# Optimization experiments

Hardware: AMD Instinct MI355X
Metric: run time of the kernel (lower is better)

The kernel has to match this reference:

```python
import jax, jax.numpy as jnp
import numpy as np

INP = 256
OUP = 256
FGROUP = 16
CGROUP = 8
K = 3
STRIDE = 1
PAD = K // 2
B, H, W = 16, 64, 64
O1 = OUP * INP * K * K // CGROUP  # 73728, glgf output channels


def setup_inputs() -> dict:
    key = jax.random.key(0)
    ks = jax.random.split(key, 11)
    s = 0.1  # keep sigmoid pre-activations in a sane range
    return {
        "x": jax.random.normal(ks[0], (B, INP, H, W), jnp.float32),
        # GLGF generating the dynamic conv weights (oup*inp*k*k//cgroup outputs)
        "g1_fc1_l": jax.random.normal(ks[1], (INP, INP // FGROUP), jnp.float32) * s,
        "g1_fc1_g1": jax.random.normal(ks[2], (FGROUP, INP // FGROUP), jnp.float32) * s,
        "g1_fc1_g2": jax.random.normal(ks[3], (INP, FGROUP), jnp.float32) * s,
        "g1_fc2_l": jax.random.normal(ks[4], (O1,), jnp.float32) * s,
        "g1_fc2_g": jax.random.normal(ks[5], (INP,), jnp.float32) * s,
        # GLGF generating the per-channel output gate c (oup outputs)
        "g2_fc1_l": jax.random.normal(ks[6], (INP, INP // FGROUP), jnp.float32) * s,
        "g2_fc1_g1": jax.random.normal(ks[7], (FGROUP, INP // FGROUP), jnp.float32) * s,
        "g2_fc1_g2": jax.random.normal(ks[8], (INP, FGROUP), jnp.float32) * s,
        "g2_fc2_l": jax.random.normal(ks[9], (OUP,), jnp.float32) * s,
        "g2_fc2_g": jax.random.normal(ks[10], (INP,), jnp.float32) * s,
    }


def glgf(g, w1l, w1g1, w1g2, w2l, w2g):
    """GLGF applied to a [B, inp] gap vector (all convs are 1x1 -> grouped linears)."""
    b, inp = g.shape
    gp = inp // FGROUP
    gg = g.reshape(b, FGROUP, gp)
    # wn_fc1_l: grouped (fgroup) inp->inp; weight [inp, inp//fgroup]
    local = jnp.einsum('bgi,goi->bgo', gg, w1l.reshape(FGROUP, gp, gp)).reshape(b, inp)
    # wn_fc1_g2(wn_fc1_g1(x)): inp->fgroup (grouped) then fgroup->inp (dense)
    glob = jnp.einsum('bgi,gi->bg', gg, w1g1) @ w1g2.T  # [b, inp]
    h = jax.nn.sigmoid(local + glob)
    # wn_fc2_l: groups=inp, inp->O; weight [O] (1 input channel per output)
    O = w2l.shape[0]
    local2 = (h[:, :, None] * w2l.reshape(inp, O // inp)).reshape(b, O)
    # wn_fc2_g: dense inp->1, broadcast-added
    glob2 = h @ w2g  # [b]
    return local2 + glob2[:, None]


def reference(x, g1_fc1_l, g1_fc1_g1, g1_fc1_g2, g1_fc2_l, g1_fc2_g,
              g2_fc1_l, g2_fc1_g1, g2_fc1_g2, g2_fc2_l, g2_fc2_g):
    b = x.shape[0]
    gap = x.mean(axis=(2, 3))  # adaptive_avg_pool2d to 1x1 -> [b, inp]
    # generate per-sample grouped conv weights: [b, oup, inp//cgroup, k, k]
    xw = glgf(gap, g1_fc1_l, g1_fc1_g1, g1_fc1_g2, g1_fc2_l, g1_fc2_g)
    w = xw.reshape(b, OUP, INP // CGROUP, K, K)
    # torch's groups=b*cgroup batch-trick == per-sample conv with groups=cgroup
    def conv_one(xi, wi):
        return jax.lax.conv_general_dilated(
            xi[None], wi, (STRIDE, STRIDE), [(PAD, PAD), (PAD, PAD)],
            feature_group_count=CGROUP,
            dimension_numbers=('NCHW', 'OIHW', 'NCHW'))[0]
    y = jax.vmap(conv_one)(x, w)  # [b, oup, H, W]
    # per-sample, per-channel gate
    c = glgf(gap, g2_fc1_l, g2_fc1_g1, g2_fc1_g2, g2_fc2_l, g2_fc2_g)  # [b, oup]
    return y * c[:, :, None, None]
```

## Files before the change

### kernel.cpp

```cpp
#include <hip/hip_runtime.h>
#include <cstddef>

typedef __attribute__((ext_vector_type(8))) short bf16x8;
typedef __attribute__((ext_vector_type(4))) unsigned short ushort4v;
typedef __attribute__((ext_vector_type(8))) unsigned short ushort8v;
typedef __attribute__((ext_vector_type(16))) float f32x16;

__device__ __forceinline__ unsigned short f2bf(float f) {
  union { float f; unsigned u; } v; v.f = f;
  unsigned r = v.u + 0x7FFFu + ((v.u >> 16) & 1u);
  return (unsigned short)(r >> 16);
}

#define PADC 132
__global__ __launch_bounds__(256) void prep_kernel(
    const float* __restrict__ x, unsigned short* __restrict__ xt,
    float* __restrict__ partials) {
  __shared__ unsigned short cm[32 * PADC];
  __shared__ float sred[32][32];
  const int bid = blockIdx.x;
  const int wkr = ((bid & 7) << 9) | (bid >> 3);
  const int yp = wkr & 31, g = (wkr >> 5) & 7, b = wkr >> 8;
  const int y0 = yp * 2;
  const int tid = threadIdx.x;
  const float* xg = x + (size_t)(b * 256 + g * 32) * 4096;

  float csum[4];
#pragma unroll
  for (int j = 0; j < 4; ++j) {
    const int idx = tid + 256 * j;
    const int ic = idx >> 5;
    const int r = idx & 31;
    const int ry = r >> 4, gx4 = (r & 15) * 4;
    const float4 v = *reinterpret_cast<const float4*>(
        xg + (size_t)ic * 4096 + (y0 + ry) * 64 + gx4);
    csum[j] = v.x + v.y + v.z + v.w;
    ushort4v s;
    s[0] = f2bf(v.x); s[1] = f2bf(v.y); s[2] = f2bf(v.z); s[3] = f2bf(v.w);
    *reinterpret_cast<ushort4v*>(&cm[ic * PADC + ry * 64 + gx4]) = s;
  }
#pragma unroll
  for (int j = 0; j < 4; ++j) {
    const int ic = (tid >> 5) + 8 * j;
    sred[ic][tid & 31] = csum[j];
  }
  __syncthreads();

  if (tid < 32) {
    float s = 0.f;
#pragma unroll
    for (int i = 0; i < 32; ++i) s += sred[tid][i];
    partials[(size_t)(b * 256 + g * 32 + tid) * 32 + yp] = s;
  }

  const size_t xtb = (size_t)(b * 8 + g) * (66 * 66 * 32);
#pragma unroll
  for (int jj = 0; jj < 2; ++jj) {
    const int o = tid + 256 * jj;
    const int px = o >> 2, icq = o & 3;
    const int ry = px >> 6, gx = px & 63;
    ushort8v t;
#pragma unroll
    for (int c2 = 0; c2 < 8; ++c2) t[c2] = cm[(icq * 8 + c2) * PADC + px];
    *reinterpret_cast<ushort8v*>(
        &xt[xtb + ((size_t)(y0 + ry + 1) * 66 + (gx + 1)) * 32 + icq * 8]) = t;
  }

  const ushort8v z = {0, 0, 0, 0, 0, 0, 0, 0};
  if (tid < 16) {
    const int rr = tid >> 3;
    const int side = (tid >> 2) & 1;
    const int icq = tid & 3;
    const int col = side * 65;
    *reinterpret_cast<ushort8v*>(
        &xt[xtb + ((size_t)(y0 + rr + 1) * 66 + col) * 32 + icq * 8]) = z;
  }
  if (yp == 0 || yp == 31) {
    const int row = (yp == 0) ? 0 : 65;
    for (int o = tid; o < 66 * 4; o += 256) {
      const int col = o >> 2, icq = o & 3;
      *reinterpret_cast<ushort8v*>(
          &xt[xtb + ((size_t)row * 66 + col) * 32 + icq * 8]) = z;
    }
  }
}

__global__ __launch_bounds__(256, 2) void conv_kernel(
    const float* __restrict__ partials,
    const float* __restrict__ w1l, const float* __restrict__ w1g1,
    const float* __restrict__ w1g2, const float* __restrict__ w2l,
    const float* __restrict__ w2g,
    const float* __restrict__ v1l, const float* __restrict__ v1g1,
    const float* __restrict__ v1g2, const float* __restrict__ v2l,
    const float* __restrict__ v2g,
    const unsigned short* __restrict__ xt, float* __restrict__ out) {
  __shared__ __align__(16) unsigned short smem[9216];
  __shared__ float gapL[256];
  __shared__ float hL[256];
  __shared__ float red[256];
  __shared__ float t1L[16];
  __shared__ float gateL[32];

  const int bid = blockIdx.x;
  const int wkr = ((bid & 7) << 7) | (bid >> 3);
  const int yq = wkr & 7;
  const int bg = wkr >> 3;
  const int g = bg & 7, b = bg >> 3;
  const int tid = threadIdx.x;
  const int c = tid;

  {
    float s = 0.f;
    const float* pp = partials + (size_t)(b * 256 + c) * 32;
#pragma unroll
    for (int i = 0; i < 32; ++i) s += pp[i];
    gapL[c] = s * (1.f / 4096.f);
  }
  __syncthreads();

  const int gbase = c & ~15;
  float local1 = 0.f;
#pragma unroll
  for (int i = 0; i < 16; ++i) local1 += gapL[gbase + i] * w1l[c * 16 + i];
  if (c < 16) {
    float t = 0.f;
#pragma unroll
    for (int i = 0; i < 16; ++i) t += gapL[c * 16 + i] * w1g1[c * 16 + i];
    t1L[c] = t;
  }
  __syncthreads();
  float glob1 = 0.f;
#pragma unroll
  for (int gg = 0; gg < 16; ++gg) glob1 += t1L[gg] * w1g2[c * 16 + gg];
  const float h1 = 1.f / (1.f + expf(-(local1 + glob1)));
  hL[c] = h1;
  red[c] = h1 * w2g[c];
  __syncthreads();
  for (int s = 128; s > 0; s >>= 1) {
    if (c < s) red[c] += red[c + s];
    __syncthreads();
  }
  const float glob2 = red[0];
  __syncthreads();

#pragma unroll 4
  for (int it = 0; it < 36; ++it) {
    const int idx = it * 256 + c;
    const int kk = idx >> 9;
    const int rem = idx & 511;
    const int l = rem >> 3, e = rem & 7;
    const int oc = l & 31, hi2 = l >> 5;
    const int ic = ((kk & 1) << 4) + hi2 * 8 + e;
    const int sp = kk >> 1;
    const int o = (g << 5) + oc;
    smem[idx] = f2bf(hL[o] * w2l[o * 288 + ic * 9 + sp] + glob2);
  }
  __syncthreads();

  float local2 = 0.f;
#pragma unroll
  for (int i = 0; i < 16; ++i) local2 += gapL[gbase + i] * v1l[c * 16 + i];
  if (c < 16) {
    float t = 0.f;
#pragma unroll
    for (int i = 0; i < 16; ++i) t += gapL[c * 16 + i] * v1g1[c * 16 + i];
    t1L[c] = t;
  }
  __syncthreads();
  float glob1b = 0.f;
#pragma unroll
  for (int gg = 0; gg < 16; ++gg) glob1b += t1L[gg] * v1g2[c * 16 + gg];
  const float h2 = 1.f / (1.f + expf(-(local2 + glob1b)));
  hL[c] = h2;
  red[c] = h2 * v2g[c];
  __syncthreads();
  for (int s = 128; s > 0; s >>= 1) {
    if (c < s) red[c] += red[c + s];
    __syncthreads();
  }
  if (c < 32) {
    const int o = g * 32 + c;
    gateL[c] = hL[o] * v2l[o] + red[0];
  }

  const int lane = tid & 63, wave = tid >> 6;
  const int n = lane & 31, hi = lane >> 5;
  const int wr = wave >> 1, wc = wave & 1;
  const size_t xtb = (size_t)bg * (66 * 66 * 32);

  bf16x8 a[18];
#pragma unroll
  for (int kk = 0; kk < 18; ++kk) {
    a[kk] = *reinterpret_cast<const bf16x8*>(&smem[kk * 512 + lane * 8]);
    asm volatile("" : "+v"(a[kk]));
  }
  __syncthreads();

  int s_live[5], s_goff[5], s_loff[5];
#pragma unroll
  for (int s = 0; s < 5; ++s) {
    const int li = s * 256 + tid;
    s_live[s] = li < 1056;
    const int r = li / 264;
    const int rem = li - r * 264;
    const int px = rem >> 2, cq = rem & 3;
    s_goff[s] = ((yq * 8 + r) * 66 + px) * 32 + cq * 8;
    s_loff[s] = (((r << 2) + (cq ^ (px & 3))) * 66 + px) * 8;
  }
  ushort8v st[5];

#pragma unroll
  for (int s = 0; s < 5; ++s)
    if (s_live[s])
      st[s] = *reinterpret_cast<const ushort8v*>(&xt[xtb + s_goff[s]]);

#pragma unroll 1
  for (int p = 0; p < 4; ++p) {
#pragma unroll
    for (int s = 0; s < 5; ++s)
      if (s_live[s])
        *reinterpret_cast<ushort8v*>(&smem[s_loff[s]]) = st[s];
    __syncthreads();

    if (p < 3) {
#pragma unroll
      for (int s = 0; s < 5; ++s)
        if (s_live[s])
          st[s] = *reinterpret_cast<const ushort8v*>(
              &xt[xtb + s_goff[s] + (p + 1) * 2 * 66 * 32]);
    }

    f32x16 acc;
#pragma unroll
    for (int i = 0; i < 16; ++i) acc[i] = 0.f;
#pragma unroll
    for (int kk = 0; kk < 18; ++kk) {
      const int sp = kk >> 1;
      const int ky = sp / 3, kx = sp % 3;
      const int px2 = wc * 32 + n + kx;
      const int cq = ((kk & 1) << 1) + hi;
      const bf16x8 bf = *reinterpret_cast<const bf16x8*>(
          &smem[((((wr + ky) << 2) + (cq ^ (px2 & 3))) * 66 + px2) * 8]);
      acc = __builtin_amdgcn_mfma_f32_32x32x16_bf16(a[kk], bf, acc, 0, 0, 0);
    }

    const int y = yq * 8 + p * 2 + wr;
    float* ob = out + (size_t)(b * 256 + g * 32) * 4096 + y * 64 + wc * 32 + n;
#pragma unroll
    for (int r = 0; r < 16; ++r) {
      const int row = (r & 3) + ((r >> 2) << 3) + (hi << 2);
      ob[(size_t)row * 4096] = acc[r] * gateL[row];
    }
    __syncthreads();
  }
}

extern "C" void kernel_launch(void* const* d_in, const int* in_sizes, int n_in,
                              void* d_out, int out_size, void* d_ws,
                              size_t ws_size, hipStream_t stream) {
  const float* x    = (const float*)d_in[0];
  const float* w1l  = (const float*)d_in[1];
  const float* w1g1 = (const float*)d_in[2];
  const float* w1g2 = (const float*)d_in[3];
  const float* w2l  = (const float*)d_in[4];
  const float* w2g  = (const float*)d_in[5];
  const float* v1l  = (const float*)d_in[6];
  const float* v1g1 = (const float*)d_in[7];
  const float* v1g2 = (const float*)d_in[8];
  const float* v2l  = (const float*)d_in[9];
  const float* v2g  = (const float*)d_in[10];
  float* out = (float*)d_out;

  unsigned short* xt = (unsigned short*)d_ws;
  float* partials = (float*)(xt + 17842176);

  prep_kernel<<<4096, 256, 0, stream>>>(x, xt, partials);
  conv_kernel<<<1024, 256, 0, stream>>>(partials, w1l, w1g1, w1g2, w2l, w2g,
                                        v1l, v1g1, v1g2, v2l, v2g, xt, out);
}
```

Measured before the change: 62.27 us.

## Split GLGF weight generation into separate kernel and slim conv kernel

Moves the GLGF weight and gate computation out of the conv kernel into a new 128-block glgf_pack kernel. Each (batch, group) pair is then computed once instead of eight times, and the gate GLGF runs once per batch. The conv kernel now copies prepacked bf16 weights into LDS, reads A fragments from LDS per MFMA instead of holding them in registers, raises the occupancy target to 4, and defers all output stores until after the four row-pair passes. This cuts redundant prologue work and register pressure at the cost of an extra launch, an LDS read per MFMA and a global round trip for the packed weights.

```diff
diff --git a/kernel.cpp b/kernel.cpp
--- a/kernel.cpp
+++ b/kernel.cpp
@@ -85,7 +85,7 @@
   }
 }
 
-__global__ __launch_bounds__(256, 2) void conv_kernel(
+__global__ __launch_bounds__(256) void glgf_pack(
     const float* __restrict__ partials,
     const float* __restrict__ w1l, const float* __restrict__ w1g1,
     const float* __restrict__ w1g2, const float* __restrict__ w2l,
@@ -93,12 +93,93 @@
     const float* __restrict__ v1l, const float* __restrict__ v1g1,
     const float* __restrict__ v1g2, const float* __restrict__ v2l,
     const float* __restrict__ v2g,
-    const unsigned short* __restrict__ xt, float* __restrict__ out) {
-  __shared__ __align__(16) unsigned short smem[9216];
+    unsigned short* __restrict__ wpack, float* __restrict__ gate) {
   __shared__ float gapL[256];
+  __shared__ float t1L[16];
   __shared__ float hL[256];
   __shared__ float red[256];
-  __shared__ float t1L[16];
+  const int bid = blockIdx.x;
+  const int bg = ((bid & 7) << 4) | (bid >> 3);
+  const int g = bg & 7, b = bg >> 3;
+  const int c = threadIdx.x;
+  {
+    float s = 0.f;
+    const float* pp = partials + (size_t)(b * 256 + c) * 32;
+#pragma unroll
+    for (int i = 0; i < 32; ++i) s += pp[i];
+    gapL[c] = s * (1.f / 4096.f);
+  }
+  __syncthreads();
+
+  const int gbase = c & ~15;
+  float local1 = 0.f;
+#pragma unroll
+  for (int i = 0; i < 16; ++i) local1 += gapL[gbase + i] * w1l[c * 16 + i];
+  if (c < 16) {
+    float t = 0.f;
+#pragma unroll
+    for (int i = 0; i < 16; ++i) t += gapL[c * 16 + i] * w1g1[c * 16 + i];
+    t1L[c] = t;
+  }
+  __syncthreads();
+  float glob1 = 0.f;
+#pragma unroll
+  for (int gg = 0; gg < 16; ++gg) glob1 += t1L[gg] * w1g2[c * 16 + gg];
+  const float h1 = 1.f / (1.f + expf(-(local1 + glob1)));
+  hL[c] = h1;
+  red[c] = h1 * w2g[c];
+  __syncthreads();
+  for (int s = 128; s > 0; s >>= 1) {
+    if (c < s) red[c] += red[c + s];
+    __syncthreads();
+  }
+  const float glob2 = red[0];
+
+  unsigned short* wpo = wpack + (size_t)bg * 9216;
+#pragma unroll 4
+  for (int it = 0; it < 36; ++it) {
+    const int idx = it * 256 + c;
+    const int kk = idx >> 9;
+    const int rem = idx & 511;
+    const int l = rem >> 3, e = rem & 7;
+    const int oc = l & 31, hi = l >> 5;
+    const int ic = ((kk & 1) << 4) + hi * 8 + e;
+    const int sp = kk >> 1;
+    const int o = (g << 5) + oc;
+    wpo[idx] = f2bf(hL[o] * w2l[o * 288 + ic * 9 + sp] + glob2);
+  }
+
+  if (g == 0) {
+    __syncthreads();
+    float local2 = 0.f;
+#pragma unroll
+    for (int i = 0; i < 16; ++i) local2 += gapL[gbase + i] * v1l[c * 16 + i];
+    if (c < 16) {
+      float t = 0.f;
+#pragma unroll
+      for (int i = 0; i < 16; ++i) t += gapL[c * 16 + i] * v1g1[c * 16 + i];
+      t1L[c] = t;
+    }
+    __syncthreads();
+    float glob1b = 0.f;
+#pragma unroll
+    for (int gg = 0; gg < 16; ++gg) glob1b += t1L[gg] * v1g2[c * 16 + gg];
+    const float h2 = 1.f / (1.f + expf(-(local2 + glob1b)));
+    red[c] = h2 * v2g[c];
+    __syncthreads();
+    for (int s = 128; s > 0; s >>= 1) {
+      if (c < s) red[c] += red[c + s];
+      __syncthreads();
+    }
+    gate[b * 256 + c] = h2 * v2l[c] + red[0];
+  }
+}
+
+__global__ __launch_bounds__(256, 4) void conv_kernel(
+    const unsigned short* __restrict__ wpack, const float* __restrict__ gate,
+    const unsigned short* __restrict__ xt, float* __restrict__ out) {
+  __shared__ __align__(16) unsigned short wpl[9216];
+  __shared__ __align__(16) unsigned short btile[8448];
   __shared__ float gateL[32];
 
   const int bid = blockIdx.x;
@@ -107,94 +188,19 @@
   const int bg = wkr >> 3;
   const int g = bg & 7, b = bg >> 3;
   const int tid = threadIdx.x;
-  const int c = tid;
-
-  {
-    float s = 0.f;
-    const float* pp = partials + (size_t)(b * 256 + c) * 32;
-#pragma unroll
-    for (int i = 0; i < 32; ++i) s += pp[i];
-    gapL[c] = s * (1.f / 4096.f);
-  }
-  __syncthreads();
-
-  const int gbase = c & ~15;
-  float local1 = 0.f;
-#pragma unroll
-  for (int i = 0; i < 16; ++i) local1 += gapL[gbase + i] * w1l[c * 16 + i];
-  if (c < 16) {
-    float t = 0.f;
-#pragma unroll
-    for (int i = 0; i < 16; ++i) t += gapL[c * 16 + i] * w1g1[c * 16 + i];
-    t1L[c] = t;
-  }
-  __syncthreads();
-  float glob1 = 0.f;
-#pragma unroll
-  for (int gg = 0; gg < 16; ++gg) glob1 += t1L[gg] * w1g2[c * 16 + gg];
-  const float h1 = 1.f / (1.f + expf(-(local1 + glob1)));
-  hL[c] = h1;
-  red[c] = h1 * w2g[c];
-  __syncthreads();
-  for (int s = 128; s > 0; s >>= 1) {
-    if (c < s) red[c] += red[c + s];
-    __syncthreads();
-  }
-  const float glob2 = red[0];
-  __syncthreads();
-
-#pragma unroll 4
-  for (int it = 0; it < 36; ++it) {
-    const int idx = it * 256 + c;
-    const int kk = idx >> 9;
-    const int rem = idx & 511;
-    const int l = rem >> 3, e = rem & 7;
-    const int oc = l & 31, hi2 = l >> 5;
-    const int ic = ((kk & 1) << 4) + hi2 * 8 + e;
-    const int sp = kk >> 1;
-    const int o = (g << 5) + oc;
-    smem[idx] = f2bf(hL[o] * w2l[o * 288 + ic * 9 + sp] + glob2);
-  }
-  __syncthreads();
-
-  float local2 = 0.f;
-#pragma unroll
-  for (int i = 0; i < 16; ++i) local2 += gapL[gbase + i] * v1l[c * 16 + i];
-  if (c < 16) {
-    float t = 0.f;
-#pragma unroll
-    for (int i = 0; i < 16; ++i) t += gapL[c * 16 + i] * v1g1[c * 16 + i];
-    t1L[c] = t;
-  }
-  __syncthreads();
-  float glob1b = 0.f;
-#pragma unroll
-  for (int gg = 0; gg < 16; ++gg) glob1b += t1L[gg] * v1g2[c * 16 + gg];
-  const float h2 = 1.f / (1.f + expf(-(local2 + glob1b)));
-  hL[c] = h2;
-  red[c] = h2 * v2g[c];
-  __syncthreads();
-  for (int s = 128; s > 0; s >>= 1) {
-    if (c < s) red[c] += red[c + s];
-    __syncthreads();
-  }
-  if (c < 32) {
-    const int o = g * 32 + c;
-    gateL[c] = hL[o] * v2l[o] + red[0];
-  }
-
-  const int lane = tid & 63, wave = tid >> 6;
+
+  const int lane = tid & 63;
   const int n = lane & 31, hi = lane >> 5;
+  const int wave = tid >> 6;
   const int wr = wave >> 1, wc = wave & 1;
   const size_t xtb = (size_t)bg * (66 * 66 * 32);
 
-  bf16x8 a[18];
-#pragma unroll
-  for (int kk = 0; kk < 18; ++kk) {
-    a[kk] = *reinterpret_cast<const bf16x8*>(&smem[kk * 512 + lane * 8]);
-    asm volatile("" : "+v"(a[kk]));
-  }
-  __syncthreads();
+  {
+    const uint4* src = reinterpret_cast<const uint4*>(wpack + (size_t)bg * 9216);
+    uint4* dst = reinterpret_cast<uint4*>(wpl);
+    for (int i = tid; i < 1152; i += 256) dst[i] = src[i];
+  }
+  if (tid < 32) gateL[tid] = gate[b * 256 + g * 32 + tid];
 
   int s_live[5], s_goff[5], s_loff[5];
 #pragma unroll
@@ -213,14 +219,21 @@
   for (int s = 0; s < 5; ++s)
     if (s_live[s])
       st[s] = *reinterpret_cast<const ushort8v*>(&xt[xtb + s_goff[s]]);
-
-#pragma unroll 1
+#pragma unroll
+  for (int s = 0; s < 5; ++s)
+    if (s_live[s]) *reinterpret_cast<ushort8v*>(&btile[s_loff[s]]) = st[s];
+
+  __syncthreads();
+
+  f32x16 acc[4];
+#pragma unroll
   for (int p = 0; p < 4; ++p) {
-#pragma unroll
-    for (int s = 0; s < 5; ++s)
-      if (s_live[s])
-        *reinterpret_cast<ushort8v*>(&smem[s_loff[s]]) = st[s];
-    __syncthreads();
+    if (p > 0) {
+#pragma unroll
+      for (int s = 0; s < 5; ++s)
+        if (s_live[s]) *reinterpret_cast<ushort8v*>(&btile[s_loff[s]]) = st[s];
+      __syncthreads();
+    }
 
     if (p < 3) {
 #pragma unroll
@@ -230,28 +243,34 @@
               &xt[xtb + s_goff[s] + (p + 1) * 2 * 66 * 32]);
     }
 
-    f32x16 acc;
-#pragma unroll
-    for (int i = 0; i < 16; ++i) acc[i] = 0.f;
+#pragma unroll
+    for (int i = 0; i < 16; ++i) acc[p][i] = 0.f;
 #pragma unroll
     for (int kk = 0; kk < 18; ++kk) {
       const int sp = kk >> 1;
       const int ky = sp / 3, kx = sp % 3;
       const int px2 = wc * 32 + n + kx;
       const int cq = ((kk & 1) << 1) + hi;
+      const bf16x8 af =
+          *reinterpret_cast<const bf16x8*>(&wpl[kk * 512 + lane * 8]);
       const bf16x8 bf = *reinterpret_cast<const bf16x8*>(
-          &smem[((((wr + ky) << 2) + (cq ^ (px2 & 3))) * 66 + px2) * 8]);
-      acc = __builtin_amdgcn_mfma_f32_32x32x16_bf16(a[kk], bf, acc, 0, 0, 0);
-    }
-
+          &btile[((((wr + ky) << 2) + (cq ^ (px2 & 3))) * 66 + px2) * 8]);
+      acc[p] = __builtin_amdgcn_mfma_f32_32x32x16_bf16(af, bf, acc[p], 0, 0, 0);
+    }
+
+    if (p < 3) __syncthreads();
+  }
+
+  float* ob0 = out + (size_t)(b * 256 + g * 32) * 4096 + wc * 32 + n;
+#pragma unroll
+  for (int p = 0; p < 4; ++p) {
     const int y = yq * 8 + p * 2 + wr;
-    float* ob = out + (size_t)(b * 256 + g * 32) * 4096 + y * 64 + wc * 32 + n;
+    float* ob = ob0 + y * 64;
 #pragma unroll
     for (int r = 0; r < 16; ++r) {
       const int row = (r & 3) + ((r >> 2) << 3) + (hi << 2);
-      ob[(size_t)row * 4096] = acc[r] * gateL[row];
-    }
-    __syncthreads();
+      ob[(size_t)row * 4096] = acc[p][r] * gateL[row];
+    }
   }
 }
 
@@ -273,8 +292,11 @@
 
   unsigned short* xt = (unsigned short*)d_ws;
   float* partials = (float*)(xt + 17842176);
+  unsigned short* wpack = (unsigned short*)(partials + 131072);
+  float* gate = (float*)(wpack + 1179648);
 
   prep_kernel<<<4096, 256, 0, stream>>>(x, xt, partials);
-  conv_kernel<<<1024, 256, 0, stream>>>(partials, w1l, w1g1, w1g2, w2l, w2g,
-                                        v1l, v1g1, v1g2, v2l, v2g, xt, out);
-}
+  glgf_pack<<<128, 256, 0, stream>>>(partials, w1l, w1g1, w1g2, w2l, w2g,
+                                     v1l, v1g1, v1g2, v2l, v2g, wpack, gate);
+  conv_kernel<<<1024, 256, 0, stream>>>(wpack, gate, xt, out);
+}
```

After: 50.59 us. -18.7%, faster.
